# Kernel optimization log

Measured on AMD Instinct MI355X. Metric: run time of the kernel, lower is better.

## Reference

```python
import jax, jax.numpy as jnp
import numpy as np

D_MODEL = 1024
N_HEADS = 16
D_HEAD = D_MODEL // N_HEADS
RANK = 16
DECAY = 0.95
ALPHA_MAX = 0.05
BETA = 0.01


def setup_inputs() -> dict:
    key = jax.random.key(0)
    ks = jax.random.split(key, 9)
    B, T = 4, 2048
    s = 0.02  # init scale for weights
    return {
        "hidden_states": jax.random.normal(ks[0], (B, T, D_MODEL), jnp.float32),
        "m_gate": jax.random.uniform(ks[1], (B, T), jnp.float32),
        "alpha_scale": jax.random.uniform(ks[2], (B, T, N_HEADS), jnp.float32),
        "Wq": jax.random.normal(ks[3], (D_MODEL, D_MODEL), jnp.float32) * s,
        "Wk": jax.random.normal(ks[4], (D_MODEL, D_MODEL), jnp.float32) * s,
        "Wv": jax.random.normal(ks[5], (D_MODEL, D_MODEL), jnp.float32) * s,
        "Wo": jax.random.normal(ks[6], (D_MODEL, D_MODEL), jnp.float32) * s,
        "Wa": jax.random.normal(ks[7], (N_HEADS, D_MODEL), jnp.float32) * s,
        "ba": jnp.zeros((N_HEADS,), jnp.float32),
        "mix_logit": jnp.zeros((N_HEADS,), jnp.float32),
    }


def reference(hidden_states, m_gate, alpha_scale, Wq, Wk, Wv, Wo, Wa, ba, mix_logit):
    B, T, D = hidden_states.shape
    H, Dh, R = N_HEADS, D_HEAD, RANK
    # batched projections (Linear: x @ W.T), then split heads
    q = (hidden_states @ Wq.T).reshape(B, T, H, Dh)
    k = (hidden_states @ Wk.T).reshape(B, T, H, Dh)
    v = (hidden_states @ Wv.T).reshape(B, T, H, Dh)
    # alpha computed under torch.no_grad in the original -> stop_gradient
    alpha = jax.nn.sigmoid(hidden_states @ Wa.T + ba)  # [B,T,H]
    alpha = alpha * m_gate[..., None] * alpha_scale
    alpha = jnp.minimum(alpha, ALPHA_MAX)
    alpha = jax.lax.stop_gradient(alpha)

    inv_sqrt_dh = 1.0 / (Dh ** 0.5)

    def step(carry, xs):
        U, V = carry  # U: [B,H,Dh,R], V: [B,H,R,Dh]
        q_t, k_t, v_t, a_t = xs  # [B,H,Dh], [B,H,Dh], [B,H,Dh], [B,H]
        U = DECAY * U
        V = DECAY * V
        ku = jnp.einsum('bhd,bhdr->bhr', k_t, U)
        a = a_t[..., None, None]
        U = U + a * jnp.einsum('bhd,bhr->bhdr', k_t, ku)
        V = V + a * jnp.einsum('bhr,bhd->bhrd', ku, v_t)
        U = U - BETA * jnp.clip(U, -1.0, 1.0)
        V = V - BETA * jnp.clip(V, -1.0, 1.0)
        # whole fast-weight update is no_grad in the original
        U = jax.lax.stop_gradient(U)
        V = jax.lax.stop_gradient(V)
        q_norm = q_t * inv_sqrt_dh
        k_fast = jnp.einsum('bhdr,bhrd->bhd', U, V)  # [B,H,Dh]
        score_slow = jnp.sum(q_norm * k_t, axis=-1)  # [B,H]
        score_fast = jnp.sum(q_norm * k_fast, axis=-1)
        logits = jnp.stack([score_slow, score_fast], axis=-1) + mix_logit[None, :, None]
        mix = jax.nn.softmax(logits, axis=-1)  # [B,H,2]
        y = mix[..., 0:1] * v_t + mix[..., 1:2] * k_fast  # [B,H,Dh]
        return (U, V), y

    U0 = jnp.zeros((B, H, Dh, R), hidden_states.dtype)
    V0 = jnp.zeros((B, H, R, Dh), hidden_states.dtype)
    xs = (jnp.moveaxis(q, 1, 0), jnp.moveaxis(k, 1, 0),
          jnp.moveaxis(v, 1, 0), jnp.moveaxis(alpha, 1, 0))
    _, ys = jax.lax.scan(step, (U0, V0), xs)  # ys: [T,B,H,Dh]
    y = jnp.moveaxis(ys, 0, 1).reshape(B, T, D)
    return y @ Wo.T
```

## Files before the change

kernel.cpp:

```cpp
#include <hip/hip_runtime.h>
#include <hip/hip_bf16.h>
#include <stdint.h>

#define D_MODEL 1024
#define N_HEADS 16
#define D_HEAD  64
#define SEQ_T   2048
#define BATCH   4

typedef unsigned short u16;
typedef __bf16 bf16x8 __attribute__((ext_vector_type(8)));
typedef float  f32x4  __attribute__((ext_vector_type(4)));

#define NT 32
#define BUF 4096
#define QNT 32

__device__ __forceinline__ u16 f2bf(float x) {
  unsigned u = __float_as_uint(x);
  u += 0x7fffu + ((u >> 16) & 1u);
  return (u16)(u >> 16);
}
__device__ __forceinline__ unsigned pk2(float a, float b) {
  return (unsigned)f2bf(a) | ((unsigned)f2bf(b) << 16);
}
__device__ __forceinline__ unsigned scale2(unsigned p, float s) {
  float lo = __uint_as_float(p << 16) * s;
  float hi = __uint_as_float(p & 0xffff0000u) * s;
  return pk2(lo, hi);
}
__device__ __forceinline__ void cp16(const u16* g, u16* l) {
  __builtin_amdgcn_global_load_lds(
      (const __attribute__((address_space(1))) unsigned int*)g,
      (__attribute__((address_space(3))) unsigned int*)l, 16, 0, 0);
}

__global__ __launch_bounds__(256) void cast_kernel(const float* __restrict__ hs,
                                                   const float* __restrict__ wq,
                                                   const float* __restrict__ wk,
                                                   const float* __restrict__ wv,
                                                   const float* __restrict__ wo,
                                                   u16* __restrict__ Xb,
                                                   u16* __restrict__ Wb) {
  int g = blockIdx.x * 256 + threadIdx.x;
  const float4* src; uint4* dst;
  if (g < (1 << 20)) {
    src = (const float4*)hs + 2 * (size_t)g;
    dst = (uint4*)Xb + g;
  } else {
    int j = g - (1 << 20);
    int R = j >> 7;
    int col8 = j & 127;
    const float* s;
    int srow;
    if (R < 2048) {
      int h = R >> 7, c = R & 127, jj = c >> 4, l = c & 15;
      srow = h * 64 + (jj >> 1) * 16 + l;
      s = (jj & 1) ? wk : wq;
    } else if (R < 3072) { s = wv; srow = R - 2048; }
    else                 { s = wo; srow = R - 3072; }
    src = (const float4*)s + (size_t)srow * 256 + col8 * 2;
    dst = (uint4*)Wb + (size_t)R * 128 + col8;
  }
  float4 lo = src[0], hi = src[1];
  uint4 o;
  o.x = pk2(lo.x, lo.y); o.y = pk2(lo.z, lo.w);
  o.z = pk2(hi.x, hi.y); o.w = pk2(hi.z, hi.w);
  *dst = o;
}

#define QVM(n) asm volatile("s_waitcnt vmcnt(" #n ")" ::: "memory")

__global__ __launch_bounds__(256, 2) void gemm_qkv_kernel(const u16* __restrict__ A,
                                                          const u16* __restrict__ B,
                                                          u16* __restrict__ Vb,
                                                          float* __restrict__ S) {
  __shared__ u16 Ls[36864];
  const int tid  = threadIdx.x;
  const int w    = tid >> 6;
  const int l    = tid & 63;
  const int quad = l >> 4;
  const int l16  = l & 15;
  const int wm   = (w >> 1) * 128;
  const int wn   = (w & 1) * 64;

  const int id  = blockIdx.y * 24 + blockIdx.x;
  const int id2 = (id & 7) * 96 + (id >> 3);
  const int bm  = id2 / 24;
  const int bn  = id2 % 24;

  const int srow = w * 16 + (l >> 2);
  const int schk = (l & 3) * 8;
  const u16* aS[4]; const u16* bS[2];
  #pragma unroll
  for (int r = 0; r < 4; ++r)
    aS[r] = A + (size_t)(bm * 256 + r * 64 + srow) * 1024 + schk;
  #pragma unroll
  for (int r = 0; r < 2; ++r)
    bS[r] = B + (size_t)(bn * 128 + r * 64 + srow) * 1024 + schk;
  u16* dA = Ls + w * 512 + l * 8;
  u16* dB = Ls + 24576 + w * 512 + l * 8;

  f32x4 acc[8][4];
  #pragma unroll
  for (int i = 0; i < 8; ++i)
    #pragma unroll
    for (int j = 0; j < 4; ++j) acc[i][j] = (f32x4){0.f, 0.f, 0.f, 0.f};

  #pragma unroll
  for (int r = 0; r < 4; ++r) cp16(aS[r] + 0 * 32, dA + 0 * 8192 + r * 2048);
  #pragma unroll
  for (int r = 0; r < 2; ++r) cp16(bS[r] + 0 * 32, dB + 0 * 4096 + r * 2048);
  #pragma unroll
  for (int r = 0; r < 4; ++r) cp16(aS[r] + 1 * 32, dA + 1 * 8192 + r * 2048);
  #pragma unroll
  for (int r = 0; r < 2; ++r) cp16(bS[r] + 1 * 32, dB + 1 * 4096 + r * 2048);
  QVM(6);
  __builtin_amdgcn_s_barrier();

  int rbuf = 0, sbuf = 2;
  #pragma unroll 1
  for (int t = 0; t < QNT; ++t) {
    if (t + 2 < QNT) {
      #pragma unroll
      for (int r = 0; r < 4; ++r)
        cp16(aS[r] + (t + 2) * 32, dA + sbuf * 8192 + r * 2048);
      #pragma unroll
      for (int r = 0; r < 2; ++r)
        cp16(bS[r] + (t + 2) * 32, dB + sbuf * 4096 + r * 2048);
    }
    const u16* Ar = Ls + rbuf * 8192;
    const u16* Br = Ls + 24576 + rbuf * 4096;
    bf16x8 af[8], bfr[4];
    #pragma unroll
    for (int i = 0; i < 8; ++i)
      af[i] = *(const bf16x8*)(Ar + (wm + i * 16 + l16) * 32 + quad * 8);
    #pragma unroll
    for (int j = 0; j < 4; ++j)
      bfr[j] = *(const bf16x8*)(Br + (wn + j * 16 + l16) * 32 + quad * 8);
    __builtin_amdgcn_s_setprio(1);
    #pragma unroll
    for (int i = 0; i < 8; ++i)
      #pragma unroll
      for (int j = 0; j < 4; ++j)
        acc[i][j] = __builtin_amdgcn_mfma_f32_16x16x32_bf16(af[i], bfr[j], acc[i][j], 0, 0, 0);
    __builtin_amdgcn_s_setprio(0);
    if (t + 2 < QNT) { QVM(6); } else { QVM(0); }
    __builtin_amdgcn_s_barrier();
    rbuf = (rbuf == 2) ? 0 : rbuf + 1;
    sbuf = (sbuf == 2) ? 0 : sbuf + 1;
  }

  if (bn < 16) {
    float part[8][4];
    #pragma unroll
    for (int i = 0; i < 8; ++i)
      #pragma unroll
      for (int e = 0; e < 4; ++e)
        part[i][e] = acc[i][0][e] * acc[i][1][e] + acc[i][2][e] * acc[i][3][e];
    #pragma unroll
    for (int m = 1; m <= 8; m <<= 1)
      #pragma unroll
      for (int i = 0; i < 8; ++i)
        #pragma unroll
        for (int e = 0; e < 4; ++e)
          part[i][e] += __shfl_xor(part[i][e], m);
    float* Sp = (float*)Ls;
    if (l16 == 0) {
      #pragma unroll
      for (int i = 0; i < 8; ++i)
        #pragma unroll
        for (int e = 0; e < 4; ++e)
          Sp[(wm + i * 16 + quad * 4 + e) * 2 + (w & 1)] = part[i][e];
    }
    __syncthreads();
    {
      int row = tid;
      float s = (Sp[row * 2] + Sp[row * 2 + 1]) * 0.125f;
      S[(size_t)(bm * 256 + row) * N_HEADS + bn] = 1.f / (1.f + __expf(-s));
    }
  } else {
    const int cb = (bn - 16) * 128;
    #pragma unroll
    for (int i = 0; i < 8; ++i)
      #pragma unroll
      for (int j = 0; j < 4; ++j)
        #pragma unroll
        for (int e = 0; e < 4; ++e) {
          int row = bm * 256 + wm + i * 16 + quad * 4 + e;
          int col = cb + wn + j * 16 + l16;
          Vb[(size_t)row * D_MODEL + col] = f2bf(acc[i][j][e]);
        }
  }
}

__global__ __launch_bounds__(256, 4) void gemm_out_kernel(const u16* __restrict__ A,
                                                          const u16* __restrict__ B,
                                                          const float* __restrict__ S,
                                                          float* __restrict__ C) {
  constexpr int K = D_MODEL, N = D_MODEL;
  __shared__ u16 As[2 * BUF];
  __shared__ u16 Bs[2 * BUF];
  const int tid  = threadIdx.x;
  const int lane = tid & 63;
  const int wave = tid >> 6;
  const int wm = (wave >> 1) * 64;
  const int wn = (wave & 1) * 64;
  const int bm = blockIdx.y * 128;
  const int bn = blockIdx.x * 128;
  const int quad = lane >> 4;
  const int l16  = lane & 15;
  const int rchunk = quad ^ ((l16 >> 1) & 3);

  const int lr = tid >> 2;
  const int lch = tid & 3;
  const int wch = lch ^ ((lr >> 1) & 3);
  const u16* Ap0 = A + (size_t)(bm + lr) * K + lch * 8;
  const u16* Ap1 = Ap0 + (size_t)64 * K;
  u16* Aw0 = As + lr * 32 + wch * 8;
  u16* Aw1 = Aw0 + 64 * 32;
  const float* Sp0 = S + (size_t)(bm + lr) * N_HEADS;
  const float* Sp1 = Sp0 + (size_t)64 * N_HEADS;

  const int srow = lane >> 2;
  const int gch  = (lane & 3) ^ ((lane >> 3) & 3);
  const u16* Bg0 = B + (size_t)(bn + wave * 16 + srow) * K + gch * 8;
  const u16* Bg1 = Bg0 + (size_t)64 * K;
  u16* Bl = Bs + wave * 16 * 32 + lane * 8;

  f32x4 acc[4][4];
  #pragma unroll
  for (int i = 0; i < 4; ++i)
    #pragma unroll
    for (int j = 0; j < 4; ++j) acc[i][j] = (f32x4){0.f, 0.f, 0.f, 0.f};

  uint4 a0 = *(const uint4*)Ap0;
  uint4 a1 = *(const uint4*)Ap1;
  float rs0 = Sp0[0], rs1 = Sp1[0];
  cp16(Bg0, Bl);           cp16(Bg1, Bl + 64 * 32);
  {
    uint4 w0, w1;
    w0.x = scale2(a0.x, rs0); w0.y = scale2(a0.y, rs0);
    w0.z = scale2(a0.z, rs0); w0.w = scale2(a0.w, rs0);
    w1.x = scale2(a1.x, rs1); w1.y = scale2(a1.y, rs1);
    w1.z = scale2(a1.z, rs1); w1.w = scale2(a1.w, rs1);
    *(uint4*)Aw0 = w0; *(uint4*)Aw1 = w1;
  }
  a0 = *(const uint4*)(Ap0 + 32);
  a1 = *(const uint4*)(Ap1 + 32);
  __syncthreads();

  #pragma unroll 2
  for (int t = 0; t < NT; ++t) {
    const int p = t & 1;
    const u16* Ar = As + p * BUF;
    const u16* Br = Bs + p * BUF;
    bf16x8 af[4], bfr[4];
    #pragma unroll
    for (int i = 0; i < 4; ++i)
      af[i] = *(const bf16x8*)(Ar + (wm + i * 16 + l16) * 32 + rchunk * 8);
    #pragma unroll
    for (int j = 0; j < 4; ++j)
      bfr[j] = *(const bf16x8*)(Br + (wn + j * 16 + l16) * 32 + rchunk * 8);
    if (t + 1 < NT) {
      const int q = (p ^ 1) * BUF;
      cp16(Bg0 + (t + 1) * 32, Bl + q);
      cp16(Bg1 + (t + 1) * 32, Bl + q + 64 * 32);
      uint4 w0, w1;
      w0.x = scale2(a0.x, rs0); w0.y = scale2(a0.y, rs0);
      w0.z = scale2(a0.z, rs0); w0.w = scale2(a0.w, rs0);
      w1.x = scale2(a1.x, rs1); w1.y = scale2(a1.y, rs1);
      w1.z = scale2(a1.z, rs1); w1.w = scale2(a1.w, rs1);
      *(uint4*)(Aw0 + q) = w0; *(uint4*)(Aw1 + q) = w1;
      if (t + 2 < NT) {
        const int o = (t + 2) * 32;
        a0 = *(const uint4*)(Ap0 + o);
        a1 = *(const uint4*)(Ap1 + o);
        rs0 = Sp0[(t + 2) >> 1];
        rs1 = Sp1[(t + 2) >> 1];
      }
    }
    #pragma unroll
    for (int i = 0; i < 4; ++i)
      #pragma unroll
      for (int j = 0; j < 4; ++j)
        acc[i][j] = __builtin_amdgcn_mfma_f32_16x16x32_bf16(af[i], bfr[j], acc[i][j], 0, 0, 0);
    __syncthreads();
  }

  #pragma unroll
  for (int i = 0; i < 4; ++i)
    #pragma unroll
    for (int j = 0; j < 4; ++j)
      #pragma unroll
      for (int e = 0; e < 4; ++e) {
        int row = bm + wm + i * 16 + quad * 4 + e;
        int col = bn + wn + j * 16 + l16;
        C[(size_t)row * N + col] = acc[i][j][e];
      }
}

extern "C" void kernel_launch(void* const* d_in, const int* in_sizes, int n_in,
                              void* d_out, int out_size, void* d_ws, size_t ws_size,
                              hipStream_t stream) {
  const float* hs = (const float*)d_in[0];
  const float* Wq = (const float*)d_in[3];
  const float* Wk = (const float*)d_in[4];
  const float* Wv = (const float*)d_in[5];
  const float* Wo = (const float*)d_in[6];

  char* ws = (char*)d_ws;
  u16*  Xb = (u16*)ws;
  u16*  Wb = (u16*)(ws + (16u << 20));
  u16*  Vb = (u16*)(ws + (24u << 20));
  float* Sb = (float*)(ws + (40u << 20));
  float* out = (float*)d_out;

  cast_kernel<<<6144, 256, 0, stream>>>(hs, Wq, Wk, Wv, Wo, Xb, Wb);
  gemm_qkv_kernel<<<dim3(24, 32), 256, 0, stream>>>(Xb, Wb, Vb, Sb);
  gemm_out_kernel<<<dim3(8, 64), 256, 0, stream>>>(
      Vb, Wb + (size_t)3072 * D_MODEL, Sb, out);
}
```

Baseline: 198.8 us.

## Shrink QKV GEMM tile to 128x128 and XOR-swizzle LDS layout

After: 206.9 us. 1.04x slower.

```diff
diff --git a/kernel.cpp b/kernel.cpp
--- a/kernel.cpp
+++ b/kernel.cpp
@@ -71,123 +71,120 @@
 
 #define QVM(n) asm volatile("s_waitcnt vmcnt(" #n ")" ::: "memory")
 
-__global__ __launch_bounds__(256, 2) void gemm_qkv_kernel(const u16* __restrict__ A,
+__global__ __launch_bounds__(256, 3) void gemm_qkv_kernel(const u16* __restrict__ A,
                                                           const u16* __restrict__ B,
                                                           u16* __restrict__ Vb,
                                                           float* __restrict__ S) {
-  __shared__ u16 Ls[36864];
+  __shared__ u16 Ls[24576];
   const int tid  = threadIdx.x;
   const int w    = tid >> 6;
   const int l    = tid & 63;
   const int quad = l >> 4;
   const int l16  = l & 15;
-  const int wm   = (w >> 1) * 128;
+  const int wm   = (w >> 1) * 64;
   const int wn   = (w & 1) * 64;
+  const int rc   = (quad ^ ((l16 >> 1) & 3)) * 8;
 
   const int id  = blockIdx.y * 24 + blockIdx.x;
-  const int id2 = (id & 7) * 96 + (id >> 3);
+  const int id2 = (id & 7) * 192 + (id >> 3);
   const int bm  = id2 / 24;
   const int bn  = id2 % 24;
 
   const int srow = w * 16 + (l >> 2);
-  const int schk = (l & 3) * 8;
-  const u16* aS[4]; const u16* bS[2];
-  #pragma unroll
-  for (int r = 0; r < 4; ++r)
-    aS[r] = A + (size_t)(bm * 256 + r * 64 + srow) * 1024 + schk;
-  #pragma unroll
-  for (int r = 0; r < 2; ++r)
-    bS[r] = B + (size_t)(bn * 128 + r * 64 + srow) * 1024 + schk;
-  u16* dA = Ls + w * 512 + l * 8;
-  u16* dB = Ls + 24576 + w * 512 + l * 8;
-
-  f32x4 acc[8][4];
-  #pragma unroll
-  for (int i = 0; i < 8; ++i)
+  const int gch  = ((l & 3) ^ ((l >> 3) & 3)) * 8;
+  const u16* aS[2]; const u16* bS[2];
+  #pragma unroll
+  for (int u = 0; u < 2; ++u) {
+    aS[u] = A + (size_t)(bm * 128 + u * 64 + srow) * 1024 + gch;
+    bS[u] = B + (size_t)(bn * 128 + u * 64 + srow) * 1024 + gch;
+  }
+  u16* dst = Ls + w * 512 + l * 8;
+
+  f32x4 acc[4][4];
+  #pragma unroll
+  for (int i = 0; i < 4; ++i)
     #pragma unroll
     for (int j = 0; j < 4; ++j) acc[i][j] = (f32x4){0.f, 0.f, 0.f, 0.f};
 
   #pragma unroll
-  for (int r = 0; r < 4; ++r) cp16(aS[r] + 0 * 32, dA + 0 * 8192 + r * 2048);
-  #pragma unroll
-  for (int r = 0; r < 2; ++r) cp16(bS[r] + 0 * 32, dB + 0 * 4096 + r * 2048);
-  #pragma unroll
-  for (int r = 0; r < 4; ++r) cp16(aS[r] + 1 * 32, dA + 1 * 8192 + r * 2048);
-  #pragma unroll
-  for (int r = 0; r < 2; ++r) cp16(bS[r] + 1 * 32, dB + 1 * 4096 + r * 2048);
-  QVM(6);
+  for (int u = 0; u < 2; ++u) cp16(aS[u] + 0, dst + u * 2048);
+  #pragma unroll
+  for (int u = 0; u < 2; ++u) cp16(bS[u] + 0, dst + 12288 + u * 2048);
+  #pragma unroll
+  for (int u = 0; u < 2; ++u) cp16(aS[u] + 32, dst + 4096 + u * 2048);
+  #pragma unroll
+  for (int u = 0; u < 2; ++u) cp16(bS[u] + 32, dst + 16384 + u * 2048);
+  QVM(4);
   __builtin_amdgcn_s_barrier();
 
   int rbuf = 0, sbuf = 2;
   #pragma unroll 1
   for (int t = 0; t < QNT; ++t) {
     if (t + 2 < QNT) {
-      #pragma unroll
-      for (int r = 0; r < 4; ++r)
-        cp16(aS[r] + (t + 2) * 32, dA + sbuf * 8192 + r * 2048);
-      #pragma unroll
-      for (int r = 0; r < 2; ++r)
-        cp16(bS[r] + (t + 2) * 32, dB + sbuf * 4096 + r * 2048);
+      const int o = (t + 2) * 32;
+      cp16(aS[0] + o, dst + sbuf * 4096);
+      cp16(aS[1] + o, dst + sbuf * 4096 + 2048);
+      cp16(bS[0] + o, dst + 12288 + sbuf * 4096);
+      cp16(bS[1] + o, dst + 12288 + sbuf * 4096 + 2048);
     }
-    const u16* Ar = Ls + rbuf * 8192;
-    const u16* Br = Ls + 24576 + rbuf * 4096;
-    bf16x8 af[8], bfr[4];
-    #pragma unroll
-    for (int i = 0; i < 8; ++i)
-      af[i] = *(const bf16x8*)(Ar + (wm + i * 16 + l16) * 32 + quad * 8);
+    const u16* Ar = Ls + rbuf * 4096;
+    const u16* Br = Ls + 12288 + rbuf * 4096;
+    bf16x8 af[4], bfr[4];
+    #pragma unroll
+    for (int i = 0; i < 4; ++i)
+      af[i] = *(const bf16x8*)(Ar + (wm + i * 16 + l16) * 32 + rc);
     #pragma unroll
     for (int j = 0; j < 4; ++j)
-      bfr[j] = *(const bf16x8*)(Br + (wn + j * 16 + l16) * 32 + quad * 8);
+      bfr[j] = *(const bf16x8*)(Br + (wn + j * 16 + l16) * 32 + rc);
     __builtin_amdgcn_s_setprio(1);
     #pragma unroll
-    for (int i = 0; i < 8; ++i)
+    for (int i = 0; i < 4; ++i)
       #pragma unroll
       for (int j = 0; j < 4; ++j)
         acc[i][j] = __builtin_amdgcn_mfma_f32_16x16x32_bf16(af[i], bfr[j], acc[i][j], 0, 0, 0);
     __builtin_amdgcn_s_setprio(0);
-    if (t + 2 < QNT) { QVM(6); } else { QVM(0); }
+    if (t + 2 < QNT) { QVM(4); } else { QVM(0); }
     __builtin_amdgcn_s_barrier();
     rbuf = (rbuf == 2) ? 0 : rbuf + 1;
     sbuf = (sbuf == 2) ? 0 : sbuf + 1;
   }
 
   if (bn < 16) {
-    float part[8][4];
-    #pragma unroll
-    for (int i = 0; i < 8; ++i)
+    float part[4][4];
+    #pragma unroll
+    for (int i = 0; i < 4; ++i)
       #pragma unroll
       for (int e = 0; e < 4; ++e)
         part[i][e] = acc[i][0][e] * acc[i][1][e] + acc[i][2][e] * acc[i][3][e];
     #pragma unroll
     for (int m = 1; m <= 8; m <<= 1)
       #pragma unroll
-      for (int i = 0; i < 8; ++i)
+      for (int i = 0; i < 4; ++i)
         #pragma unroll
         for (int e = 0; e < 4; ++e)
           part[i][e] += __shfl_xor(part[i][e], m);
     float* Sp = (float*)Ls;
     if (l16 == 0) {
       #pragma unroll
-      for (int i = 0; i < 8; ++i)
+      for (int i = 0; i < 4; ++i)
         #pragma unroll
         for (int e = 0; e < 4; ++e)
           Sp[(wm + i * 16 + quad * 4 + e) * 2 + (w & 1)] = part[i][e];
     }
     __syncthreads();
-    {
-      int row = tid;
-      float s = (Sp[row * 2] + Sp[row * 2 + 1]) * 0.125f;
-      S[(size_t)(bm * 256 + row) * N_HEADS + bn] = 1.f / (1.f + __expf(-s));
+    if (tid < 128) {
+      float s = (Sp[tid * 2] + Sp[tid * 2 + 1]) * 0.125f;
+      S[(size_t)(bm * 128 + tid) * N_HEADS + bn] = 1.f / (1.f + __expf(-s));
     }
   } else {
     const int cb = (bn - 16) * 128;
     #pragma unroll
-    for (int i = 0; i < 8; ++i)
+    for (int i = 0; i < 4; ++i)
       #pragma unroll
       for (int j = 0; j < 4; ++j)
         #pragma unroll
         for (int e = 0; e < 4; ++e) {
-          int row = bm * 256 + wm + i * 16 + quad * 4 + e;
+          int row = bm * 128 + wm + i * 16 + quad * 4 + e;
           int col = cb + wn + j * 16 + l16;
           Vb[(size_t)row * D_MODEL + col] = f2bf(acc[i][j][e]);
         }
@@ -317,7 +314,7 @@
   float* out = (float*)d_out;
 
   cast_kernel<<<6144, 256, 0, stream>>>(hs, Wq, Wk, Wv, Wo, Xb, Wb);
-  gemm_qkv_kernel<<<dim3(24, 32), 256, 0, stream>>>(Xb, Wb, Vb, Sb);
+  gemm_qkv_kernel<<<dim3(24, 64), 256, 0, stream>>>(Xb, Wb, Vb, Sb);
   gemm_out_kernel<<<dim3(8, 64), 256, 0, stream>>>(
       Vb, Wb + (size_t)3072 * D_MODEL, Sb, out);
 }
```
